# Performance work log

Hardware: AMD Instinct MI355X
Metric: run time of the kernel (lower is better)

The kernel has to match this reference:

```python
import jax, jax.numpy as jnp
import numpy as np

TGT_LEN = 1024
MEM_LEN = 1024
SAME_LENGTH = True
D_MODEL = 2048
BATCH = 4


def _make_ft_real(tgt_len: int, mem_len: int, same_length: bool) -> jnp.ndarray:
    """Build the banded Fourier mixing matrix. Since the module's input x is real
    and only .real of the output is returned, Re(FT @ x) == Re(FT) @ x, so we
    precompute only the real part (this also matches the kernel-headroom note:
    the imaginary output is never used)."""
    qlen = tgt_len
    klen = tgt_len + mem_len
    flen = klen - qlen + 1
    m = np.outer(np.arange(qlen), np.arange(flen))
    ft = np.exp(2j * np.pi * m / flen) / np.sqrt(flen)  # [qlen, flen] complex
    ft = np.pad(ft, ((0, 0), (klen - flen, 0)))          # left-pad to [qlen, klen]
    for i in range(qlen):  # setup-time numpy loop over fixed qlen rows (not traced)
        ft[i] = np.roll(ft[i], -(qlen - i - 1))
    ft = np.tril(ft, klen - qlen)
    if same_length:
        ft = np.triu(ft, 0)
    return jnp.asarray(ft.real.astype(np.float32))


_FT_REAL = _make_ft_real(TGT_LEN, MEM_LEN, SAME_LENGTH)  # [tgt_len, tgt_len+mem_len]


def setup_inputs() -> dict:
    key = jax.random.key(0)
    k1, k2 = jax.random.split(key)
    klen = TGT_LEN + MEM_LEN
    x = jax.random.normal(k1, (BATCH, klen, D_MODEL), dtype=jnp.float32)
    p = jax.random.normal(k2, (BATCH, klen, D_MODEL), dtype=jnp.float32)
    return {"x": x, "p": p, "qlen": TGT_LEN, "add_position": 1}


def reference(x, p, qlen, add_position):
    # Dropout is identity in eval mode (deterministic reference).
    if add_position:
        x = x + p
    klen = x.shape[1]
    ft = _FT_REAL[-qlen:, -klen:]                    # [qlen, klen]
    scale = np.float32(1.0 / np.sqrt(klen))
    # Banded token-mixing matmul; real part only (x is real).
    out = jnp.einsum("lm,bmd->bld", ft, x) * scale   # [B, qlen, D]
    return out
```

## Files before the change

kernel.cpp:

```cpp
#include <hip/hip_runtime.h>
#include <hip/hip_bf16.h>
#include <cstdint>

#define QLEN   1024
#define KLEN   2048
#define DMODEL 2048
#define BATCH  4
#define FLEN   (KLEN - QLEN + 1)

typedef __bf16 bf16x8 __attribute__((ext_vector_type(8)));
typedef float  f32x4  __attribute__((ext_vector_type(4)));

__device__ __align__(16) __bf16 g_ft[(size_t)QLEN * KLEN];
__device__ __align__(16) __bf16 g_yt[(size_t)BATCH * DMODEL * KLEN];

typedef __attribute__((address_space(1))) void gvoid;
typedef __attribute__((address_space(3))) void svoid;

__device__ __forceinline__ void async_load16(const void* g, void* lds) {
  gvoid* gp = (gvoid*)(uintptr_t)g;
  svoid* sp = (svoid*)(uint32_t)(uintptr_t)lds;
  __builtin_amdgcn_global_load_lds(gp, sp, 16, 0, 0);
}

#define YT_UNITS (BATCH * (KLEN / 8) * (DMODEL / 64))
#define FT_UNITS ((QLEN * KLEN) / 512)
#define PREP_BLOCKS 1536

__global__ __launch_bounds__(256) void prep_kernel(const float* __restrict__ x,
                                                   const float* __restrict__ p,
                                                   const int* __restrict__ addp,
                                                   __bf16* __restrict__ ftp,
                                                   __bf16* __restrict__ ytp) {
  __bf16* ft = ftp ? ftp : g_ft;
  __bf16* yt = ytp ? ytp : g_yt;
  const int lane  = threadIdx.x & 63;
  const int gw    = (blockIdx.x * 256 + threadIdx.x) >> 6;
  const int nw    = PREP_BLOCKS * 4;
  const int doadd = *addp;

  for (int u = gw; u < YT_UNITS + FT_UNITS; u += nw) {
    if (u < YT_UNITS) {
      const int b  = u >> 13;
      const int r5 = u & 8191;
      const int mt = r5 >> 5;
      const int db = r5 & 31;
      const int d  = db * 64 + lane;
      const float* xp = x + ((size_t)b * KLEN + mt * 8) * DMODEL + d;
      float v[8];
#pragma unroll
      for (int i = 0; i < 8; ++i) v[i] = xp[(size_t)i * DMODEL];
      if (doadd) {
        const float* pp = p + ((size_t)b * KLEN + mt * 8) * DMODEL + d;
#pragma unroll
        for (int i = 0; i < 8; ++i) v[i] += pp[(size_t)i * DMODEL];
      }
      bf16x8 o;
#pragma unroll
      for (int i = 0; i < 8; ++i) o[i] = (__bf16)v[i];
      *(bf16x8*)(yt + ((size_t)b * (KLEN / 8) * DMODEL + (size_t)mt * DMODEL + d) * 8) = o;
    } else {
      const int uu = (u - YT_UNITS) * 64 + lane;
      const int l  = uu >> 8;
      const int m0 = (uu & 255) * 8;
      const int j0 = m0 - l;
      bf16x8 o = {};
      if (j0 + 7 >= 0 && j0 < FLEN) {
        const float w     = 6.283185307179586f / (float)FLEN;
        const float scale = 1.0f / sqrtf((float)FLEN * (float)KLEN);
#pragma unroll
        for (int i = 0; i < 8; ++i) {
          const int j = j0 + i;
          float vv = 0.0f;
          if (j >= 0 && j < FLEN) {
            const int rr = (l * j) % FLEN;
            vv = cosf((float)rr * w) * scale;
          }
          o[i] = (__bf16)vv;
        }
      }
      *(bf16x8*)(ft + (size_t)uu * 8) = o;
    }
  }
}

#define BM 128
#define BN 128
#define BK 64

__global__ __launch_bounds__(256) void gemm_kernel(float* __restrict__ out,
                                                   const __bf16* __restrict__ ftq,
                                                   const __bf16* __restrict__ ytq) {
  __shared__ __align__(16) __bf16 As[BM * BK];
  __shared__ __align__(16) __bf16 Bs[BN * BK];
  const int flat = blockIdx.x;
  const int swz  = (flat & 7) * 64 + (flat >> 3);
  const int bn = swz & 15, bm = (swz >> 4) & 7, b = swz >> 7;
  const int l0 = bm * BM, d0 = bn * BN;
  const int tid  = threadIdx.x;
  const int lane = tid & 63;
  const int wave = tid >> 6;
  const int wr = wave >> 1, wc = wave & 1;
  const int col = lane & 15, quad = lane >> 4;

  f32x4 acc[4][4] = {};

  const int t0 = l0 >> 6;
  const int t1 = (l0 + BM - 1 + FLEN - 1) >> 6;
  const __bf16* ftp = ftq ? ftq : g_ft;
  const __bf16* ytp = (ytq ? ytq : g_yt) + (size_t)b * DMODEL * KLEN;

  for (int t = t0; t <= t1; ++t) {
    const int k0 = t * BK;
#pragma unroll
    for (int s = 0; s < 4; ++s) {
      const int cb  = wave * 256 + s * 64;
      const int lc  = cb + lane;
      const int row = lc >> 3;
      const int gc8 = (lc & 7) ^ (row & 7);
      async_load16(ftp + (size_t)(l0 + row) * KLEN + k0 + gc8 * 8, As + cb * 8);
    }
#pragma unroll
    for (int s = 0; s < 4; ++s) {
      const int idx = wave * 256 + s * 64 + lane;
      const int c   = idx >> 7;
      const int dd  = idx & 127;
      async_load16(ytp + ((size_t)(t * 8 + c) * DMODEL + (d0 + dd)) * 8, Bs + (size_t)idx * 8);
    }
    __syncthreads();

#pragma unroll
    for (int kk = 0; kk < 2; ++kk) {
      bf16x8 af[4], bq[4];
      const int c8 = kk * 4 + quad;
#pragma unroll
      for (int ti = 0; ti < 4; ++ti) {
        const int r = wr * 64 + ti * 16 + col;
        af[ti] = *(const bf16x8*)(As + (size_t)((r << 3) + (c8 ^ (r & 7))) * 8);
      }
#pragma unroll
      for (int tj = 0; tj < 4; ++tj) {
        const int r = wc * 64 + tj * 16 + col;
        bq[tj] = *(const bf16x8*)(Bs + (size_t)((c8 << 7) + r) * 8);
      }
#pragma unroll
      for (int ti = 0; ti < 4; ++ti)
#pragma unroll
        for (int tj = 0; tj < 4; ++tj)
          acc[ti][tj] = __builtin_amdgcn_mfma_f32_16x16x32_bf16(af[ti], bq[tj], acc[ti][tj], 0, 0, 0);
    }
    __syncthreads();
  }

#pragma unroll
  for (int ti = 0; ti < 4; ++ti) {
    const int l = l0 + wr * 64 + ti * 16 + quad * 4;
#pragma unroll
    for (int tj = 0; tj < 4; ++tj) {
      const int d = d0 + wc * 64 + tj * 16 + col;
      float* op = out + (size_t)b * QLEN * DMODEL + (size_t)l * DMODEL + d;
#pragma unroll
      for (int r2 = 0; r2 < 4; ++r2) op[(size_t)r2 * DMODEL] = acc[ti][tj][r2];
    }
  }
}

extern "C" void kernel_launch(void* const* d_in, const int* in_sizes, int n_in,
                              void* d_out, int out_size, void* d_ws, size_t ws_size,
                              hipStream_t stream) {
  const float* x   = (const float*)d_in[0];
  const float* p   = (const float*)d_in[1];
  const int* addp  = (const int*)d_in[3];
  float* out = (float*)d_out;

  const size_t FT_BYTES = (size_t)QLEN * KLEN * sizeof(__bf16);
  const size_t YT_BYTES = (size_t)BATCH * DMODEL * KLEN * sizeof(__bf16);
  __bf16* ft = nullptr;
  __bf16* yt = nullptr;
  char* ws = (char*)d_ws;
  if (ws && ws_size >= FT_BYTES + YT_BYTES) {
    ft = (__bf16*)ws;
    yt = (__bf16*)(ws + FT_BYTES);
  } else if (ws && ws_size >= YT_BYTES) {
    yt = (__bf16*)ws;
  }

  prep_kernel<<<dim3(PREP_BLOCKS), dim3(256), 0, stream>>>(x, p, addp, ft, yt);
  gemm_kernel<<<dim3(512), dim3(256), 0, stream>>>(out, ft, yt);
}
```

Baseline: 189.1 us.

## Transpose-pack prep through LDS with vectorized row loads, one block per tile

The prep kernel now gives each block an 8-row slab of x+p. It reads contiguous float4s per row, converts them to bf16 into a padded LDS buffer, then writes the interleaved 8-wide bf16 layout with 16-byte stores. The earlier version had each lane do strided scalar loads across rows. The launch moves from a grid-stride loop to one block per unit, giving 1024 transpose blocks plus 1024 Fourier-matrix blocks. This should make the large fp32 read (~134MB) more coalesced, at the cost of LDS use and a barrier per block.

New measurement: 194.1 us. 1.03x slower.

```diff
diff --git a/kernel.cpp b/kernel.cpp
--- a/kernel.cpp
+++ b/kernel.cpp
@@ -9,6 +9,7 @@
 #define FLEN   (KLEN - QLEN + 1)
 
 typedef __bf16 bf16x8 __attribute__((ext_vector_type(8)));
+typedef __bf16 bf16x4 __attribute__((ext_vector_type(4)));
 typedef float  f32x4  __attribute__((ext_vector_type(4)));
 
 __device__ __align__(16) __bf16 g_ft[(size_t)QLEN * KLEN];
@@ -23,64 +24,73 @@
   __builtin_amdgcn_global_load_lds(gp, sp, 16, 0, 0);
 }
 
-#define YT_UNITS (BATCH * (KLEN / 8) * (DMODEL / 64))
-#define FT_UNITS ((QLEN * KLEN) / 512)
-#define PREP_BLOCKS 1536
+#define PITCH 2080
 
 __global__ __launch_bounds__(256) void prep_kernel(const float* __restrict__ x,
                                                    const float* __restrict__ p,
                                                    const int* __restrict__ addp,
                                                    __bf16* __restrict__ ftp,
                                                    __bf16* __restrict__ ytp) {
+  __shared__ __align__(16) __bf16 rows[8 * PITCH];
   __bf16* ft = ftp ? ftp : g_ft;
   __bf16* yt = ytp ? ytp : g_yt;
-  const int lane  = threadIdx.x & 63;
-  const int gw    = (blockIdx.x * 256 + threadIdx.x) >> 6;
-  const int nw    = PREP_BLOCKS * 4;
-  const int doadd = *addp;
-
-  for (int u = gw; u < YT_UNITS + FT_UNITS; u += nw) {
-    if (u < YT_UNITS) {
-      const int b  = u >> 13;
-      const int r5 = u & 8191;
-      const int mt = r5 >> 5;
-      const int db = r5 & 31;
-      const int d  = db * 64 + lane;
-      const float* xp = x + ((size_t)b * KLEN + mt * 8) * DMODEL + d;
-      float v[8];
-#pragma unroll
-      for (int i = 0; i < 8; ++i) v[i] = xp[(size_t)i * DMODEL];
-      if (doadd) {
-        const float* pp = p + ((size_t)b * KLEN + mt * 8) * DMODEL + d;
-#pragma unroll
-        for (int i = 0; i < 8; ++i) v[i] += pp[(size_t)i * DMODEL];
-      }
+  const int tid  = threadIdx.x;
+  const int lane = tid & 63;
+  const int wave = tid >> 6;
+
+  if (blockIdx.x < BATCH * (KLEN / 8)) {
+    const int b  = blockIdx.x >> 8;
+    const int mt = blockIdx.x & 255;
+    const int doadd = *addp;
+#pragma unroll
+    for (int r = 0; r < 2; ++r) {
+      const int i = wave * 2 + r;
+      const float* xr = x + ((size_t)b * KLEN + mt * 8 + i) * DMODEL;
+      const float* pr = p + ((size_t)b * KLEN + mt * 8 + i) * DMODEL;
+#pragma unroll
+      for (int s = 0; s < 8; ++s) {
+        f32x4 v = *(const f32x4*)(xr + s * 256 + lane * 4);
+        if (doadd) {
+          f32x4 q = *(const f32x4*)(pr + s * 256 + lane * 4);
+          v = v + q;
+        }
+        bf16x4 o;
+#pragma unroll
+        for (int j = 0; j < 4; ++j) o[j] = (__bf16)v[j];
+        *(bf16x4*)(rows + (size_t)i * PITCH + s * 256 + lane * 4) = o;
+      }
+    }
+    __syncthreads();
+    __bf16* outp = yt + ((size_t)b * 256 + mt) * (size_t)(2048 * 8);
+#pragma unroll
+    for (int s = 0; s < 8; ++s) {
+      const int c = s * 256 + tid;
       bf16x8 o;
 #pragma unroll
-      for (int i = 0; i < 8; ++i) o[i] = (__bf16)v[i];
-      *(bf16x8*)(yt + ((size_t)b * (KLEN / 8) * DMODEL + (size_t)mt * DMODEL + d) * 8) = o;
-    } else {
-      const int uu = (u - YT_UNITS) * 64 + lane;
-      const int l  = uu >> 8;
-      const int m0 = (uu & 255) * 8;
-      const int j0 = m0 - l;
-      bf16x8 o = {};
-      if (j0 + 7 >= 0 && j0 < FLEN) {
-        const float w     = 6.283185307179586f / (float)FLEN;
-        const float scale = 1.0f / sqrtf((float)FLEN * (float)KLEN);
-#pragma unroll
-        for (int i = 0; i < 8; ++i) {
-          const int j = j0 + i;
-          float vv = 0.0f;
-          if (j >= 0 && j < FLEN) {
-            const int rr = (l * j) % FLEN;
-            vv = cosf((float)rr * w) * scale;
-          }
-          o[i] = (__bf16)vv;
+      for (int i = 0; i < 8; ++i) o[i] = rows[(size_t)i * PITCH + c];
+      *(bf16x8*)(outp + (size_t)c * 8) = o;
+    }
+  } else {
+    const int uu = (blockIdx.x - BATCH * (KLEN / 8)) * 256 + tid;
+    const int l  = uu >> 8;
+    const int m0 = (uu & 255) * 8;
+    const int j0 = m0 - l;
+    bf16x8 o = {};
+    if (j0 + 7 >= 0 && j0 < FLEN) {
+      const float w     = 6.283185307179586f / (float)FLEN;
+      const float scale = 1.0f / sqrtf((float)FLEN * (float)KLEN);
+#pragma unroll
+      for (int i = 0; i < 8; ++i) {
+        const int j = j0 + i;
+        float vv = 0.0f;
+        if (j >= 0 && j < FLEN) {
+          const int rr = (l * j) % FLEN;
+          vv = cosf((float)rr * w) * scale;
         }
-      }
-      *(bf16x8*)(ft + (size_t)uu * 8) = o;
-    }
+        o[i] = (__bf16)vv;
+      }
+    }
+    *(bf16x8*)(ft + (size_t)uu * 8) = o;
   }
 }
 
@@ -185,6 +195,6 @@
     yt = (__bf16*)ws;
   }
 
-  prep_kernel<<<dim3(PREP_BLOCKS), dim3(256), 0, stream>>>(x, p, addp, ft, yt);
+  prep_kernel<<<dim3(BATCH * (KLEN / 8) + (QLEN * KLEN / 8) / 256), dim3(256), 0, stream>>>(x, p, addp, ft, yt);
   gemm_kernel<<<dim3(512), dim3(256), 0, stream>>>(out, ft, yt);
 }
```
